# Performance work log

Hardware: AMD Instinct MI355X
Metric: run time of the kernel (lower is better)

Reference implementation:

```python
import jax, jax.numpy as jnp
import numpy as np
import math

L, B, S, D, H, FF = 6, 4, 1024, 1024, 16, 4096
HD = D // H
EPS = 1e-5


def _ln(x, g, b):
    m = jnp.mean(x, axis=-1, keepdims=True)
    v = jnp.mean(jnp.square(x - m), axis=-1, keepdims=True)
    return (x - m) / jnp.sqrt(v + EPS) * g + b


def setup_inputs() -> dict:
    key = jax.random.key(0)
    ks = jax.random.split(key, 8)
    std = 0.02
    inp = {
        'x': jax.random.normal(ks[0], (B, S, D), jnp.float32),
        'lengths': jax.random.randint(ks[1], (B,), S // 2, S + 1),
        'rel_bias': jax.random.normal(ks[2], (H, S, S), jnp.float32) * std,
        'ln1_g': jnp.ones((L, D), jnp.float32),
        'ln1_b': jnp.zeros((L, D), jnp.float32),
        'qkv_w': jax.random.normal(ks[3], (L, D, 3 * D), jnp.float32) * std,
        'qkv_b': jnp.zeros((L, 3 * D), jnp.float32),
        'out_w': jax.random.normal(ks[4], (L, D, D), jnp.float32) * std,
        'out_b': jnp.zeros((L, D), jnp.float32),
        'ln2_g': jnp.ones((L, D), jnp.float32),
        'ln2_b': jnp.zeros((L, D), jnp.float32),
        'fc1_w': jax.random.normal(ks[5], (L, D, FF), jnp.float32) * std,
        'fc1_b': jnp.zeros((L, FF), jnp.float32),
        'fc2_w': jax.random.normal(ks[6], (L, FF, D), jnp.float32) * std,
        'fc2_b': jnp.zeros((L, D), jnp.float32),
    }
    return inp


def reference(x, lengths, rel_bias, ln1_g, ln1_b, qkv_w, qkv_b, out_w, out_b,
              ln2_g, ln2_b, fc1_w, fc1_b, fc2_w, fc2_b):
    # causal additive mask [S,S]: -inf above the diagonal (torch.triu diagonal=1)
    ar = jnp.arange(S)
    causal = jnp.where(ar[None, :] > ar[:, None], -jnp.inf, 0.0).astype(x.dtype)
    # key padding mask [B,S]: True where position is padding
    pad = ar[None, :] >= lengths[:, None]
    scale = 1.0 / math.sqrt(HD)

    for i in range(L):
        # --- attention sub-block (pre-LN) ---
        xn = _ln(x, ln1_g[i], ln1_b[i])
        qkv = xn @ qkv_w[i] + qkv_b[i]                      # [B,S,3D]
        q, k, v = jnp.split(qkv, 3, axis=-1)
        q = q.reshape(B, S, H, HD)
        k = k.reshape(B, S, H, HD)
        v = v.reshape(B, S, H, HD)
        scores = jnp.einsum('bqhd,bkhd->bhqk', q, k) * scale  # [B,H,S,S]
        scores = scores + rel_bias[None] + causal[None, None]
        scores = jnp.where(pad[:, None, None, :], -jnp.inf, scores)
        attn = jax.nn.softmax(scores, axis=-1)
        o = jnp.einsum('bhqk,bkhd->bqhd', attn, v).reshape(B, S, D)
        o = o @ out_w[i] + out_b[i]
        o = jnp.where(pad[:, :, None], 0.0, o)
        x = x + o
        # --- feed-forward sub-block (LN inside FF, residual outside) ---
        h = _ln(x, ln2_g[i], ln2_b[i])
        h = jax.nn.gelu(h @ fc1_w[i] + fc1_b[i], approximate=False)
        h = h @ fc2_w[i] + fc2_b[i]
        x = x + h
    return x
```

## Files before the change

### kernel.cpp

```cpp
#include <hip/hip_runtime.h>
#include <cstdint>
#include <cstddef>

constexpr int L_ = 6, B_ = 4, S_ = 1024, D_ = 1024, H_ = 16, FF_ = 4096;
constexpr int D3_ = 3 * D_;
constexpr int HD_ = D_ / H_;

typedef float f32x4 __attribute__((ext_vector_type(4)));
typedef __bf16 bf16x8 __attribute__((ext_vector_type(8)));
typedef unsigned short u16;
typedef u16 u16x4 __attribute__((ext_vector_type(4)));
typedef u16 u16x8 __attribute__((ext_vector_type(8)));

__device__ __forceinline__ u16 f2bf(float f) {
    union { float f; uint32_t u; } v; v.f = f;
    uint32_t r = v.u + 0x7FFFu + ((v.u >> 16) & 1u);
    return (u16)(r >> 16);
}

__device__ __forceinline__ void gload16(const void* g, void* l) {
    __builtin_amdgcn_global_load_lds(
        (const __attribute__((address_space(1))) unsigned int*)g,
        (__attribute__((address_space(3))) unsigned int*)l,
        16, 0, 0);
}

__global__ __launch_bounds__(256) void cvt_layer(
    const float* __restrict__ qw, const float* __restrict__ ow,
    const float* __restrict__ f1w, const float* __restrict__ f2w,
    u16* __restrict__ tq, u16* __restrict__ to,
    u16* __restrict__ t1, u16* __restrict__ t2)
{
    __shared__ float tile[64][65];
    const int bid = blockIdx.x, tid = threadIdx.x;
    const float* W; u16* WT; int K, N, bn, bk;
    if (bid < 768)       { W = qw;  WT = tq; K = 1024; N = 3072; int t = bid;        bn = (t % 48) * 64; bk = (t / 48) * 64; }
    else if (bid < 1024) { W = ow;  WT = to; K = 1024; N = 1024; int t = bid - 768;  bn = (t % 16) * 64; bk = (t / 16) * 64; }
    else if (bid < 2048) { W = f1w; WT = t1; K = 1024; N = 4096; int t = bid - 1024; bn = (t % 64) * 64; bk = (t / 64) * 64; }
    else                 { W = f2w; WT = t2; K = 4096; N = 1024; int t = bid - 2048; bn = (t % 16) * 64; bk = (t / 16) * 64; }
    #pragma unroll
    for (int i = 0; i < 16; ++i) {
        int idx = i * 256 + tid;
        int r = idx >> 6, c = idx & 63;
        tile[r][c] = W[(size_t)(bk + r) * N + bn + c];
    }
    __syncthreads();
    #pragma unroll
    for (int i = 0; i < 16; ++i) {
        int idx = i * 256 + tid;
        int r = idx >> 6, c = idx & 63;
        WT[(size_t)(bn + r) * K + bk + c] = f2bf(tile[c][r]);
    }
}

__global__ __launch_bounds__(256) void vt_transpose(
    const u16* __restrict__ qkv, u16* __restrict__ vt)
{
    __shared__ u16 tile[64][72];
    const int tid = threadIdx.x;
    const int s0 = blockIdx.x * 64, bh = blockIdx.y;
    const int b = bh >> 4, h = bh & 15;
    #pragma unroll
    for (int i = 0; i < 2; ++i) {
        int idx = tid + i * 256;
        int r = idx >> 3, c8 = (idx & 7) * 8;
        u16x8 v = *(const u16x8*)(qkv + ((size_t)(b * S_ + s0 + r)) * D3_ + 2 * D_ + h * 64 + c8);
        #pragma unroll
        for (int j = 0; j < 8; ++j) tile[c8 + j][r] = v[j];
    }
    __syncthreads();
    #pragma unroll
    for (int i = 0; i < 2; ++i) {
        int idx = tid + i * 256;
        int r = idx >> 3, c8 = (idx & 7) * 8;
        u16x8 v;
        #pragma unroll
        for (int j = 0; j < 8; ++j) v[j] = tile[r][c8 + j];
        *(u16x8*)(vt + ((size_t)(bh * 64 + r)) * S_ + s0 + c8) = v;
    }
}

__global__ __launch_bounds__(256) void ln_kernel(
    const float* __restrict__ X, const float* __restrict__ g,
    const float* __restrict__ bp, u16* __restrict__ out)
{
    const int row = blockIdx.x, tid = threadIdx.x;
    const float* xr = X + (size_t)row * D_;
    f32x4 v = *(const f32x4*)(xr + tid * 4);
    float s  = v[0] + v[1] + v[2] + v[3];
    float s2 = v[0]*v[0] + v[1]*v[1] + v[2]*v[2] + v[3]*v[3];
    #pragma unroll
    for (int off = 32; off >= 1; off >>= 1) {
        s  += __shfl_down(s,  off);
        s2 += __shfl_down(s2, off);
    }
    __shared__ float red[8];
    const int lane = tid & 63, wid = tid >> 6;
    if (lane == 0) { red[wid] = s; red[4 + wid] = s2; }
    __syncthreads();
    s  = red[0] + red[1] + red[2] + red[3];
    s2 = red[4] + red[5] + red[6] + red[7];
    float mean = s * (1.f / D_);
    float var  = s2 * (1.f / D_) - mean * mean;
    float rstd = rsqrtf(var + 1e-5f);
    f32x4 gv = *(const f32x4*)(g  + tid * 4);
    f32x4 bv = *(const f32x4*)(bp + tid * 4);
    u16x4 o4;
    #pragma unroll
    for (int r = 0; r < 4; ++r) o4[r] = f2bf((v[r] - mean) * rstd * gv[r] + bv[r]);
    *(u16x4*)(out + (size_t)row * D_ + tid * 4) = o4;
}

template<int MODE>
__global__ __launch_bounds__(512, 2) void gemm256d(
    const u16* __restrict__ A, const u16* __restrict__ BT,
    const float* __restrict__ bias,
    u16* __restrict__ Cb, float* __restrict__ X,
    const int* __restrict__ lengths,
    int M, int N, int K)
{
    __shared__ __align__(16) char lds[4][32768];
    const int tid = threadIdx.x;
    const int lane = tid & 63;
    const int w = tid >> 6;
    const int grp = lane >> 4, l15 = lane & 15;
    const int wm = w >> 2, wn = w & 3;
    const int m0 = blockIdx.y * 256, n0 = blockIdx.x * 256;
    const int Kh = K / gridDim.z;
    const int k0 = blockIdx.z * Kh;
    const int NT = Kh >> 5;

    const int lrow = lane >> 2;
    const int cchunk = (lane & 3) ^ ((lane >> 3) & 3);
    const u16* gA = A  + (size_t)(m0 + w * 32 + lrow) * K + k0 + cchunk * 8;
    const u16* gB = BT + (size_t)(n0 + w * 32 + lrow) * K + k0 + cchunk * 8;
    const size_t row16 = (size_t)16 * K;
    char* const lA = &lds[0][0]     + w * 2048;
    char* const lB = &lds[0][16384] + w * 2048;
    const int rslot = (grp ^ ((l15 >> 1) & 3)) * 16;

#define STAGE_A(t) do { const u16* p_ = gA + (size_t)(t) * 32;                 \
        char* l_ = lA + ((t) & 3) * 32768;                                     \
        gload16(p_, l_); gload16(p_ + row16, l_ + 1024); } while (0)
#define STAGE_B(t) do { const u16* p_ = gB + (size_t)(t) * 32;                 \
        char* l_ = lB + ((t) & 3) * 32768;                                     \
        gload16(p_, l_); gload16(p_ + row16, l_ + 1024); } while (0)

    f32x4 acc[8][4] = {};

    STAGE_A(0); STAGE_B(0);
    if (NT > 1) { STAGE_A(1); STAGE_B(1); }
    if (NT > 2) { STAGE_A(2); STAGE_B(2); }

    for (int t = 0; t < NT; ++t) {
        const int rem = NT - t;
        if (rem > 2)       asm volatile("s_waitcnt vmcnt(8)" ::: "memory");
        else if (rem == 2) asm volatile("s_waitcnt vmcnt(4)" ::: "memory");
        else               asm volatile("s_waitcnt vmcnt(0)" ::: "memory");
        __builtin_amdgcn_s_barrier();
        __builtin_amdgcn_sched_barrier(0);
        const char* Ab = &lds[t & 3][0];
        const char* Bb = &lds[t & 3][16384];

        bf16x8 bfr[4], af0[4], af1[4];
        #pragma unroll
        for (int nf = 0; nf < 4; ++nf)
            bfr[nf] = *(const bf16x8*)(Bb + (wn * 64 + nf * 16 + l15) * 64 + rslot);
        #pragma unroll
        for (int mf = 0; mf < 4; ++mf)
            af0[mf] = *(const bf16x8*)(Ab + (wm * 128 + mf * 16 + l15) * 64 + rslot);
        if (t + 3 < NT) STAGE_A(t + 3);
        __builtin_amdgcn_s_setprio(1);
        #pragma unroll
        for (int mf = 0; mf < 4; ++mf)
            #pragma unroll
            for (int nf = 0; nf < 4; ++nf)
                acc[mf][nf] = __builtin_amdgcn_mfma_f32_16x16x32_bf16(
                    af0[mf], bfr[nf], acc[mf][nf], 0, 0, 0);
        __builtin_amdgcn_s_setprio(0);
        #pragma unroll
        for (int mf = 0; mf < 4; ++mf)
            af1[mf] = *(const bf16x8*)(Ab + (wm * 128 + 64 + mf * 16 + l15) * 64 + rslot);
        if (t + 3 < NT) STAGE_B(t + 3);
        __builtin_amdgcn_s_setprio(1);
        #pragma unroll
        for (int mf = 0; mf < 4; ++mf)
            #pragma unroll
            for (int nf = 0; nf < 4; ++nf)
                acc[4 + mf][nf] = __builtin_amdgcn_mfma_f32_16x16x32_bf16(
                    af1[mf], bfr[nf], acc[4 + mf][nf], 0, 0, 0);
        __builtin_amdgcn_s_setprio(0);
    }
#undef STAGE_A
#undef STAGE_B

    const float bscale = (k0 == 0) ? 1.f : 0.f;
    #pragma unroll
    for (int mi = 0; mi < 8; ++mi) {
        int row_g = m0 + wm * 128 + mi * 16 + grp * 4;
        #pragma unroll
        for (int nf = 0; nf < 4; ++nf) {
            int col_g = n0 + wn * 64 + nf * 16 + l15;
            float bv = bias[col_g] * bscale;
            f32x4 v = acc[mi][nf];
            if constexpr (MODE == 0) {
                #pragma unroll
                for (int r = 0; r < 4; ++r)
                    Cb[(size_t)(row_g + r) * N + col_g] = f2bf(v[r] + bv);
            } else if constexpr (MODE == 2) {
                #pragma unroll
                for (int r = 0; r < 4; ++r) {
                    float t = v[r] + bv;
                    float ge = 0.5f * t * (1.f + erff(t * 0.70710678118654752f));
                    Cb[(size_t)(row_g + r) * N + col_g] = f2bf(ge);
                }
            } else if constexpr (MODE == 1) {
                int len = lengths[row_g >> 10];
                #pragma unroll
                for (int r = 0; r < 4; ++r) {
                    int row = row_g + r;
                    float add = ((row & 1023) >= len) ? 0.f : (v[r] + bv);
                    atomicAdd(&X[(size_t)row * N + col_g], add);
                }
            } else {
                #pragma unroll
                for (int r = 0; r < 4; ++r)
                    atomicAdd(&X[(size_t)(row_g + r) * N + col_g], v[r] + bv);
            }
        }
    }
}

__global__ __launch_bounds__(256) void attn_kernel(
    const u16* __restrict__ qkv,
    const u16* __restrict__ vt,
    const float* __restrict__ rel_bias,
    const int* __restrict__ lengths,
    u16* __restrict__ obuf)
{
    __shared__ __align__(16) char kls[64 * 128];
    __shared__ __align__(16) char vls[64 * 128];
    const int tid = threadIdx.x, lane = tid & 63, wid = tid >> 6;
    const int grp = lane >> 4, l15 = lane & 15;
    const int qt = blockIdx.x, bh = blockIdx.y;
    const int b = bh >> 4, h = bh & 15;
    const int len = lengths[b];
    const int qrow = qt * 64 + wid * 16 + l15;

    bf16x8 qf[2];
    {
        const u16* qp = qkv + ((size_t)(b * S_ + qrow)) * D3_ + h * 64 + grp * 8;
        qf[0] = *(const bf16x8*)qp;
        qf[1] = *(const bf16x8*)(qp + 32);
    }
    f32x4 oacc[4] = {};
    float m_run = -INFINITY, lsum = 0.f;
    int kt_end = (len + 63) >> 6;
    if (qt + 1 < kt_end) kt_end = qt + 1;

    for (int kt = 0; kt < kt_end; ++kt) {
        __syncthreads();
        #pragma unroll
        for (int i = 0; i < 2; ++i) {
            int id2 = tid + i * 256;
            int r = id2 >> 3, gg = id2 & 7;
            int sw = (r & 7) << 4;
            bf16x8 kv = *(const bf16x8*)(qkv + ((size_t)(b * S_ + kt * 64 + r)) * D3_ + D_ + h * 64 + gg * 8);
            *(bf16x8*)(kls + r * 128 + ((gg * 16) ^ sw)) = kv;
            bf16x8 vv = *(const bf16x8*)(vt + ((size_t)(bh * 64 + r)) * S_ + kt * 64 + gg * 8);
            *(bf16x8*)(vls + r * 128 + ((gg * 16) ^ sw)) = vv;
        }
        __syncthreads();

        f32x4 sf[4] = {};
        #pragma unroll
        for (int f = 0; f < 4; ++f) {
            int r = f * 16 + l15;
            int sw = (r & 7) << 4;
            #pragma unroll
            for (int t = 0; t < 2; ++t) {
                bf16x8 af = *(const bf16x8*)(kls + r * 128 + (((t * 32 + grp * 8) * 2) ^ sw));
                sf[f] = __builtin_amdgcn_mfma_f32_16x16x32_bf16(af, qf[t], sf[f], 0, 0, 0);
            }
        }
        float p[4][4];
        float tmax = -INFINITY;
        #pragma unroll
        for (int f = 0; f < 4; ++f) {
            f32x4 bi = *(const f32x4*)(rel_bias + ((size_t)h * S_ + qrow) * S_ + kt * 64 + f * 16 + grp * 4);
            #pragma unroll
            for (int r = 0; r < 4; ++r) {
                int kp = kt * 64 + f * 16 + grp * 4 + r;
                bool valid = (kp <= qrow) && (kp < len);
                float sv = valid ? fmaf(sf[f][r], 0.125f, bi[r]) : -INFINITY;
                p[f][r] = sv;
                tmax = fmaxf(tmax, sv);
            }
        }
        tmax = fmaxf(tmax, __shfl_xor(tmax, 16));
        tmax = fmaxf(tmax, __shfl_xor(tmax, 32));
        float m_new = fmaxf(m_run, tmax);
        float alpha = expf(m_run - m_new);
        float psum = 0.f;
        #pragma unroll
        for (int f = 0; f < 4; ++f)
            #pragma unroll
            for (int r = 0; r < 4; ++r) {
                float e = expf(p[f][r] - m_new);
                p[f][r] = e; psum += e;
            }
        psum += __shfl_xor(psum, 16);
        psum += __shfl_xor(psum, 32);
        lsum = lsum * alpha + psum;
        m_run = m_new;
        #pragma unroll
        for (int fo = 0; fo < 4; ++fo) {
            oacc[fo][0] *= alpha; oacc[fo][1] *= alpha;
            oacc[fo][2] *= alpha; oacc[fo][3] *= alpha;
        }
        #pragma unroll
        for (int t = 0; t < 2; ++t) {
            union { u16 u[8]; bf16x8 v; } pb;
            #pragma unroll
            for (int j = 0; j < 4; ++j) {
                pb.u[j]     = f2bf(p[2 * t][j]);
                pb.u[4 + j] = f2bf(p[2 * t + 1][j]);
            }
            #pragma unroll
            for (int fo = 0; fo < 4; ++fo) {
                int r = fo * 16 + l15;
                int sw = (r & 7) << 4;
                union { u16x4 h4[2]; bf16x8 v; } av;
                av.h4[0] = *(const u16x4*)(vls + r * 128 + ((t * 64 + grp * 8)      ^ sw));
                av.h4[1] = *(const u16x4*)(vls + r * 128 + ((t * 64 + grp * 8 + 32) ^ sw));
                oacc[fo] = __builtin_amdgcn_mfma_f32_16x16x32_bf16(av.v, pb.v, oacc[fo], 0, 0, 0);
            }
        }
    }
    float inv = 1.f / lsum;
    #pragma unroll
    for (int fo = 0; fo < 4; ++fo)
        #pragma unroll
        for (int r = 0; r < 4; ++r) {
            int hd = fo * 16 + grp * 4 + r;
            obuf[((size_t)(b * S_) + qrow) * D_ + h * 64 + hd] = f2bf(oacc[fo][r] * inv);
        }
}

extern "C" void kernel_launch(void* const* d_in, const int* in_sizes, int n_in,
                              void* d_out, int out_size, void* d_ws, size_t ws_size,
                              hipStream_t stream)
{
    const float* x_in     = (const float*)d_in[0];
    const int*   lengths  = (const int*)d_in[1];
    const float* rel_bias = (const float*)d_in[2];
    const float* ln1_g    = (const float*)d_in[3];
    const float* ln1_b    = (const float*)d_in[4];
    const float* qkv_w    = (const float*)d_in[5];
    const float* qkv_b    = (const float*)d_in[6];
    const float* out_w    = (const float*)d_in[7];
    const float* out_b    = (const float*)d_in[8];
    const float* ln2_g    = (const float*)d_in[9];
    const float* ln2_b    = (const float*)d_in[10];
    const float* fc1_w    = (const float*)d_in[11];
    const float* fc1_b    = (const float*)d_in[12];
    const float* fc2_w    = (const float*)d_in[13];
    const float* fc2_b    = (const float*)d_in[14];
    float* X = (float*)d_out;

    char* ws = (char*)d_ws;
    size_t off = 0;
    auto alloc = [&](size_t bytes) {
        char* p = ws + off;
        off = (off + bytes + 255) & ~(size_t)255;
        return p;
    };
    u16* wT_qkv = (u16*)alloc((size_t)D3_ * D_ * 2);
    u16* wT_out = (u16*)alloc((size_t)D_ * D_ * 2);
    u16* wT_fc1 = (u16*)alloc((size_t)FF_ * D_ * 2);
    u16* wT_fc2 = (u16*)alloc((size_t)D_ * FF_ * 2);
    u16* xn     = (u16*)alloc((size_t)B_ * S_ * D_ * 2);
    u16* qkvb   = (u16*)alloc((size_t)B_ * S_ * D3_ * 2);
    u16* vtb    = (u16*)alloc((size_t)B_ * H_ * HD_ * S_ * 2);
    u16* ob     = (u16*)alloc((size_t)B_ * S_ * D_ * 2);
    u16* h1     = (u16*)alloc((size_t)B_ * S_ * FF_ * 2);

    const int M = B_ * S_;

    hipMemcpyAsync(X, x_in, (size_t)M * D_ * sizeof(float),
                   hipMemcpyDeviceToDevice, stream);

    for (int i = 0; i < L_; ++i) {
        cvt_layer<<<3072, 256, 0, stream>>>(
            qkv_w + (size_t)i * D_ * D3_, out_w + (size_t)i * D_ * D_,
            fc1_w + (size_t)i * D_ * FF_, fc2_w + (size_t)i * FF_ * D_,
            wT_qkv, wT_out, wT_fc1, wT_fc2);

        ln_kernel<<<M, 256, 0, stream>>>(X, ln1_g + i * D_, ln1_b + i * D_, xn);
        gemm256d<0><<<dim3(D3_ / 256, M / 256, 1), 512, 0, stream>>>(
            xn, wT_qkv, qkv_b + (size_t)i * D3_, qkvb, nullptr, nullptr, M, D3_, D_);
        vt_transpose<<<dim3(S_ / 64, B_ * H_), 256, 0, stream>>>(qkvb, vtb);
        attn_kernel<<<dim3(S_ / 64, B_ * H_), 256, 0, stream>>>(
            qkvb, vtb, rel_bias, lengths, ob);
        gemm256d<1><<<dim3(D_ / 256, M / 256, 4), 512, 0, stream>>>(
            ob, wT_out, out_b + (size_t)i * D_, nullptr, X, lengths, M, D_, D_);

        ln_kernel<<<M, 256, 0, stream>>>(X, ln2_g + i * D_, ln2_b + i * D_, xn);
        gemm256d<2><<<dim3(FF_ / 256, M / 256, 1), 512, 0, stream>>>(
            xn, wT_fc1, fc1_b + (size_t)i * FF_, h1, nullptr, nullptr, M, FF_, D_);
        gemm256d<3><<<dim3(D_ / 256, M / 256, 4), 512, 0, stream>>>(
            h1, wT_fc2, fc2_b + (size_t)i * D_, nullptr, X, nullptr, M, D_, FF_);
    }
}
```

Before: 1.929 ms.

## Unroll GEMM K-loop over four static LDS buffers and remap workgroups per XCD

```diff
diff --git a/kernel.cpp b/kernel.cpp
--- a/kernel.cpp
+++ b/kernel.cpp
@@ -112,22 +112,39 @@
 }
 
 template<int MODE>
-__global__ __launch_bounds__(512, 2) void gemm256d(
+__global__ __launch_bounds__(512, 2) void gemm256p(
     const u16* __restrict__ A, const u16* __restrict__ BT,
     const float* __restrict__ bias,
     u16* __restrict__ Cb, float* __restrict__ X,
     const int* __restrict__ lengths,
     int M, int N, int K)
 {
-    __shared__ __align__(16) char lds[4][32768];
+    __shared__ __align__(16) char sb0[32768];
+    __shared__ __align__(16) char sb1[32768];
+    __shared__ __align__(16) char sb2[32768];
+    __shared__ __align__(16) char sb3[32768];
+
     const int tid = threadIdx.x;
     const int lane = tid & 63;
     const int w = tid >> 6;
     const int grp = lane >> 4, l15 = lane & 15;
     const int wm = w >> 2, wn = w & 3;
-    const int m0 = blockIdx.y * 256, n0 = blockIdx.x * 256;
+
+    const int gx = gridDim.x, gy = gridDim.y;
+    const int nwg = gx * gy * gridDim.z;
+    int lid = blockIdx.x + gx * (blockIdx.y + gy * blockIdx.z);
+    {
+        int q = nwg >> 3, r = nwg & 7;
+        int xcd = lid & 7, wi = lid >> 3;
+        lid = (xcd < r ? xcd * (q + 1) : r * (q + 1) + (xcd - r) * q) + wi;
+    }
+    const int bx = lid % gx;
+    const int byz = lid / gx;
+    const int by = byz % gy, bz = byz / gy;
+
+    const int m0 = by * 256, n0 = bx * 256;
     const int Kh = K / gridDim.z;
-    const int k0 = blockIdx.z * Kh;
+    const int k0 = bz * Kh;
     const int NT = Kh >> 5;
 
     const int lrow = lane >> 2;
@@ -135,64 +152,68 @@
     const u16* gA = A  + (size_t)(m0 + w * 32 + lrow) * K + k0 + cchunk * 8;
     const u16* gB = BT + (size_t)(n0 + w * 32 + lrow) * K + k0 + cchunk * 8;
     const size_t row16 = (size_t)16 * K;
-    char* const lA = &lds[0][0]     + w * 2048;
-    char* const lB = &lds[0][16384] + w * 2048;
     const int rslot = (grp ^ ((l15 >> 1) & 3)) * 16;
 
-#define STAGE_A(t) do { const u16* p_ = gA + (size_t)(t) * 32;                 \
-        char* l_ = lA + ((t) & 3) * 32768;                                     \
-        gload16(p_, l_); gload16(p_ + row16, l_ + 1024); } while (0)
-#define STAGE_B(t) do { const u16* p_ = gB + (size_t)(t) * 32;                 \
-        char* l_ = lB + ((t) & 3) * 32768;                                     \
-        gload16(p_, l_); gload16(p_ + row16, l_ + 1024); } while (0)
+#define STAGE(t, BUF) do {                                                    \
+        const u16* pa_ = gA + (size_t)(t) * 32;                               \
+        const u16* pb_ = gB + (size_t)(t) * 32;                               \
+        char* la_ = (BUF) + w * 2048;                                         \
+        char* lb_ = (BUF) + 16384 + w * 2048;                                 \
+        gload16(pa_, la_); gload16(pa_ + row16, la_ + 1024);                  \
+        gload16(pb_, lb_); gload16(pb_ + row16, lb_ + 1024); } while (0)
 
     f32x4 acc[8][4] = {};
 
-    STAGE_A(0); STAGE_B(0);
-    if (NT > 1) { STAGE_A(1); STAGE_B(1); }
-    if (NT > 2) { STAGE_A(2); STAGE_B(2); }
-
-    for (int t = 0; t < NT; ++t) {
-        const int rem = NT - t;
-        if (rem > 2)       asm volatile("s_waitcnt vmcnt(8)" ::: "memory");
-        else if (rem == 2) asm volatile("s_waitcnt vmcnt(4)" ::: "memory");
-        else               asm volatile("s_waitcnt vmcnt(0)" ::: "memory");
-        __builtin_amdgcn_s_barrier();
-        __builtin_amdgcn_sched_barrier(0);
-        const char* Ab = &lds[t & 3][0];
-        const char* Bb = &lds[t & 3][16384];
-
-        bf16x8 bfr[4], af0[4], af1[4];
-        #pragma unroll
-        for (int nf = 0; nf < 4; ++nf)
-            bfr[nf] = *(const bf16x8*)(Bb + (wn * 64 + nf * 16 + l15) * 64 + rslot);
-        #pragma unroll
-        for (int mf = 0; mf < 4; ++mf)
-            af0[mf] = *(const bf16x8*)(Ab + (wm * 128 + mf * 16 + l15) * 64 + rslot);
-        if (t + 3 < NT) STAGE_A(t + 3);
-        __builtin_amdgcn_s_setprio(1);
-        #pragma unroll
-        for (int mf = 0; mf < 4; ++mf)
-            #pragma unroll
-            for (int nf = 0; nf < 4; ++nf)
-                acc[mf][nf] = __builtin_amdgcn_mfma_f32_16x16x32_bf16(
-                    af0[mf], bfr[nf], acc[mf][nf], 0, 0, 0);
-        __builtin_amdgcn_s_setprio(0);
-        #pragma unroll
-        for (int mf = 0; mf < 4; ++mf)
-            af1[mf] = *(const bf16x8*)(Ab + (wm * 128 + 64 + mf * 16 + l15) * 64 + rslot);
-        if (t + 3 < NT) STAGE_B(t + 3);
-        __builtin_amdgcn_s_setprio(1);
-        #pragma unroll
-        for (int mf = 0; mf < 4; ++mf)
-            #pragma unroll
-            for (int nf = 0; nf < 4; ++nf)
-                acc[4 + mf][nf] = __builtin_amdgcn_mfma_f32_16x16x32_bf16(
-                    af1[mf], bfr[nf], acc[4 + mf][nf], 0, 0, 0);
-        __builtin_amdgcn_s_setprio(0);
-    }
-#undef STAGE_A
-#undef STAGE_B
+#define TILEBODY(CUR, WAITSTR, STAGE_STMT) do {                               \
+        asm volatile(WAITSTR ::: "memory");                                   \
+        __builtin_amdgcn_s_barrier();                                         \
+        __builtin_amdgcn_sched_barrier(0);                                    \
+        const char* Ab_ = (CUR);                                              \
+        const char* Bb_ = (CUR) + 16384;                                      \
+        bf16x8 bfr_[4], af0_[4], af1_[4];                                     \
+        _Pragma("unroll")                                                     \
+        for (int nf = 0; nf < 4; ++nf)                                        \
+            bfr_[nf] = *(const bf16x8*)(Bb_ + (wn * 64 + nf * 16 + l15) * 64 + rslot); \
+        _Pragma("unroll")                                                     \
+        for (int mf = 0; mf < 4; ++mf)                                        \
+            af0_[mf] = *(const bf16x8*)(Ab_ + (wm * 128 + mf * 16 + l15) * 64 + rslot); \
+        _Pragma("unroll")                                                     \
+        for (int mf = 0; mf < 4; ++mf)                                        \
+            af1_[mf] = *(const bf16x8*)(Ab_ + (wm * 128 + 64 + mf * 16 + l15) * 64 + rslot); \
+        STAGE_STMT;                                                           \
+        __builtin_amdgcn_s_setprio(1);                                        \
+        _Pragma("unroll")                                                     \
+        for (int mf = 0; mf < 4; ++mf)                                        \
+            _Pragma("unroll")                                                 \
+            for (int nf = 0; nf < 4; ++nf)                                    \
+                acc[mf][nf] = __builtin_amdgcn_mfma_f32_16x16x32_bf16(        \
+                    af0_[mf], bfr_[nf], acc[mf][nf], 0, 0, 0);                \
+        _Pragma("unroll")                                                     \
+        for (int mf = 0; mf < 4; ++mf)                                        \
+            _Pragma("unroll")                                                 \
+            for (int nf = 0; nf < 4; ++nf)                                    \
+                acc[4 + mf][nf] = __builtin_amdgcn_mfma_f32_16x16x32_bf16(    \
+                    af1_[mf], bfr_[nf], acc[4 + mf][nf], 0, 0, 0);            \
+        __builtin_amdgcn_s_setprio(0);                                        \
+    } while (0)
+
+    STAGE(0, sb0);
+    STAGE(1, sb1);
+    STAGE(2, sb2);
+
+    int t = 0;
+    for (; t + 4 < NT; t += 4) {
+        TILEBODY(sb0, "s_waitcnt vmcnt(8)", STAGE(t + 3, sb3));
+        TILEBODY(sb1, "s_waitcnt vmcnt(8)", STAGE(t + 4, sb0));
+        TILEBODY(sb2, "s_waitcnt vmcnt(8)", STAGE(t + 5, sb1));
+        TILEBODY(sb3, "s_waitcnt vmcnt(8)", STAGE(t + 6, sb2));
+    }
+    TILEBODY(sb0, "s_waitcnt vmcnt(8)", STAGE(t + 3, sb3));
+    TILEBODY(sb1, "s_waitcnt vmcnt(8)", (void)0);
+    TILEBODY(sb2, "s_waitcnt vmcnt(4)", (void)0);
+    TILEBODY(sb3, "s_waitcnt vmcnt(0)", (void)0);
+#undef TILEBODY
+#undef STAGE
 
     const float bscale = (k0 == 0) ? 1.f : 0.f;
     #pragma unroll
@@ -210,8 +231,8 @@
             } else if constexpr (MODE == 2) {
                 #pragma unroll
                 for (int r = 0; r < 4; ++r) {
-                    float t = v[r] + bv;
-                    float ge = 0.5f * t * (1.f + erff(t * 0.70710678118654752f));
+                    float tv = v[r] + bv;
+                    float ge = 0.5f * tv * (1.f + erff(tv * 0.70710678118654752f));
                     Cb[(size_t)(row_g + r) * N + col_g] = f2bf(ge);
                 }
             } else if constexpr (MODE == 1) {
@@ -397,18 +418,18 @@
             wT_qkv, wT_out, wT_fc1, wT_fc2);
 
         ln_kernel<<<M, 256, 0, stream>>>(X, ln1_g + i * D_, ln1_b + i * D_, xn);
-        gemm256d<0><<<dim3(D3_ / 256, M / 256, 1), 512, 0, stream>>>(
+        gemm256p<0><<<dim3(D3_ / 256, M / 256, 1), 512, 0, stream>>>(
             xn, wT_qkv, qkv_b + (size_t)i * D3_, qkvb, nullptr, nullptr, M, D3_, D_);
         vt_transpose<<<dim3(S_ / 64, B_ * H_), 256, 0, stream>>>(qkvb, vtb);
         attn_kernel<<<dim3(S_ / 64, B_ * H_), 256, 0, stream>>>(
             qkvb, vtb, rel_bias, lengths, ob);
-        gemm256d<1><<<dim3(D_ / 256, M / 256, 4), 512, 0, stream>>>(
+        gemm256p<1><<<dim3(D_ / 256, M / 256, 4), 512, 0, stream>>>(
             ob, wT_out, out_b + (size_t)i * D_, nullptr, X, lengths, M, D_, D_);
 
         ln_kernel<<<M, 256, 0, stream>>>(X, ln2_g + i * D_, ln2_b + i * D_, xn);
-        gemm256d<2><<<dim3(FF_ / 256, M / 256, 1), 512, 0, stream>>>(
+        gemm256p<2><<<dim3(FF_ / 256, M / 256, 1), 512, 0, stream>>>(
             xn, wT_fc1, fc1_b + (size_t)i * FF_, h1, nullptr, nullptr, M, FF_, D_);
-        gemm256d<3><<<dim3(D_ / 256, M / 256, 4), 512, 0, stream>>>(
+        gemm256p<3><<<dim3(D_ / 256, M / 256, 4), 512, 0, stream>>>(
             h1, wT_fc2, fc2_b + (size_t)i * D_, nullptr, X, nullptr, M, D_, FF_);
     }
 }
```

Measured after the change: 1.904 ms. Within noise of the previous version (-1.3%).

## Remap GEMM workgroups per XCD and restructure pipeline into barrier-fenced phases

Applied to the files above, without the earlier changes.

```diff
diff --git a/kernel.cpp b/kernel.cpp
--- a/kernel.cpp
+++ b/kernel.cpp
@@ -112,7 +112,7 @@
 }
 
 template<int MODE>
-__global__ __launch_bounds__(512, 2) void gemm256d(
+__global__ __launch_bounds__(512, 2) void gemm8p(
     const u16* __restrict__ A, const u16* __restrict__ BT,
     const float* __restrict__ bias,
     u16* __restrict__ Cb, float* __restrict__ X,
@@ -125,9 +125,22 @@
     const int w = tid >> 6;
     const int grp = lane >> 4, l15 = lane & 15;
     const int wm = w >> 2, wn = w & 3;
-    const int m0 = blockIdx.y * 256, n0 = blockIdx.x * 256;
+
+    const int gx = gridDim.x, gy = gridDim.y;
+    const int nwg = gx * gy * gridDim.z;
+    int lid = blockIdx.x + gx * (blockIdx.y + gy * blockIdx.z);
+    {
+        int q = nwg >> 3, r = nwg & 7;
+        int xcd = lid & 7, wi = lid >> 3;
+        lid = (xcd < r ? xcd * (q + 1) : r * (q + 1) + (xcd - r) * q) + wi;
+    }
+    const int bx = lid % gx;
+    const int byz = lid / gx;
+    const int by = byz % gy, bz = byz / gy;
+
+    const int m0 = by * 256, n0 = bx * 256;
     const int Kh = K / gridDim.z;
-    const int k0 = blockIdx.z * Kh;
+    const int k0 = bz * Kh;
     const int NT = Kh >> 5;
 
     const int lrow = lane >> 2;
@@ -135,61 +148,67 @@
     const u16* gA = A  + (size_t)(m0 + w * 32 + lrow) * K + k0 + cchunk * 8;
     const u16* gB = BT + (size_t)(n0 + w * 32 + lrow) * K + k0 + cchunk * 8;
     const size_t row16 = (size_t)16 * K;
-    char* const lA = &lds[0][0]     + w * 2048;
-    char* const lB = &lds[0][16384] + w * 2048;
     const int rslot = (grp ^ ((l15 >> 1) & 3)) * 16;
 
-#define STAGE_A(t) do { const u16* p_ = gA + (size_t)(t) * 32;                 \
-        char* l_ = lA + ((t) & 3) * 32768;                                     \
+#define STAGE_A(t) do { const u16* p_ = gA + (size_t)(t) * 32;                \
+        char* l_ = &lds[(t) & 3][0] + w * 2048;                               \
         gload16(p_, l_); gload16(p_ + row16, l_ + 1024); } while (0)
-#define STAGE_B(t) do { const u16* p_ = gB + (size_t)(t) * 32;                 \
-        char* l_ = lB + ((t) & 3) * 32768;                                     \
+#define STAGE_B(t) do { const u16* p_ = gB + (size_t)(t) * 32;                \
+        char* l_ = &lds[(t) & 3][16384] + w * 2048;                           \
         gload16(p_, l_); gload16(p_ + row16, l_ + 1024); } while (0)
 
     f32x4 acc[8][4] = {};
 
     STAGE_A(0); STAGE_B(0);
-    if (NT > 1) { STAGE_A(1); STAGE_B(1); }
-    if (NT > 2) { STAGE_A(2); STAGE_B(2); }
+    STAGE_A(1); STAGE_B(1);
+    STAGE_A(2); STAGE_B(2);
+    asm volatile("s_waitcnt vmcnt(8)" ::: "memory");
+    __builtin_amdgcn_s_barrier();
 
     for (int t = 0; t < NT; ++t) {
-        const int rem = NT - t;
-        if (rem > 2)       asm volatile("s_waitcnt vmcnt(8)" ::: "memory");
-        else if (rem == 2) asm volatile("s_waitcnt vmcnt(4)" ::: "memory");
-        else               asm volatile("s_waitcnt vmcnt(0)" ::: "memory");
-        __builtin_amdgcn_s_barrier();
-        __builtin_amdgcn_sched_barrier(0);
         const char* Ab = &lds[t & 3][0];
         const char* Bb = &lds[t & 3][16384];
-
-        bf16x8 bfr[4], af0[4], af1[4];
+        bf16x8 bfr[4], af[4];
+
         #pragma unroll
         for (int nf = 0; nf < 4; ++nf)
             bfr[nf] = *(const bf16x8*)(Bb + (wn * 64 + nf * 16 + l15) * 64 + rslot);
         #pragma unroll
         for (int mf = 0; mf < 4; ++mf)
-            af0[mf] = *(const bf16x8*)(Ab + (wm * 128 + mf * 16 + l15) * 64 + rslot);
+            af[mf] = *(const bf16x8*)(Ab + (wm * 128 + mf * 16 + l15) * 64 + rslot);
         if (t + 3 < NT) STAGE_A(t + 3);
+        __builtin_amdgcn_s_barrier();
+        asm volatile("s_waitcnt lgkmcnt(0)" ::: "memory");
+        __builtin_amdgcn_sched_barrier(0);
         __builtin_amdgcn_s_setprio(1);
         #pragma unroll
         for (int mf = 0; mf < 4; ++mf)
             #pragma unroll
             for (int nf = 0; nf < 4; ++nf)
                 acc[mf][nf] = __builtin_amdgcn_mfma_f32_16x16x32_bf16(
-                    af0[mf], bfr[nf], acc[mf][nf], 0, 0, 0);
+                    af[mf], bfr[nf], acc[mf][nf], 0, 0, 0);
         __builtin_amdgcn_s_setprio(0);
+        __builtin_amdgcn_s_barrier();
+
         #pragma unroll
         for (int mf = 0; mf < 4; ++mf)
-            af1[mf] = *(const bf16x8*)(Ab + (wm * 128 + 64 + mf * 16 + l15) * 64 + rslot);
+            af[mf] = *(const bf16x8*)(Ab + (wm * 128 + 64 + mf * 16 + l15) * 64 + rslot);
         if (t + 3 < NT) STAGE_B(t + 3);
+        if (t + 3 < NT)      asm volatile("s_waitcnt vmcnt(8)" ::: "memory");
+        else if (t + 2 < NT) asm volatile("s_waitcnt vmcnt(4)" ::: "memory");
+        else                 asm volatile("s_waitcnt vmcnt(0)" ::: "memory");
+        __builtin_amdgcn_s_barrier();
+        asm volatile("s_waitcnt lgkmcnt(0)" ::: "memory");
+        __builtin_amdgcn_sched_barrier(0);
         __builtin_amdgcn_s_setprio(1);
         #pragma unroll
         for (int mf = 0; mf < 4; ++mf)
             #pragma unroll
             for (int nf = 0; nf < 4; ++nf)
                 acc[4 + mf][nf] = __builtin_amdgcn_mfma_f32_16x16x32_bf16(
-                    af1[mf], bfr[nf], acc[4 + mf][nf], 0, 0, 0);
+                    af[mf], bfr[nf], acc[4 + mf][nf], 0, 0, 0);
         __builtin_amdgcn_s_setprio(0);
+        __builtin_amdgcn_s_barrier();
     }
 #undef STAGE_A
 #undef STAGE_B
@@ -210,8 +229,8 @@
             } else if constexpr (MODE == 2) {
                 #pragma unroll
                 for (int r = 0; r < 4; ++r) {
-                    float t = v[r] + bv;
-                    float ge = 0.5f * t * (1.f + erff(t * 0.70710678118654752f));
+                    float tv = v[r] + bv;
+                    float ge = 0.5f * tv * (1.f + erff(tv * 0.70710678118654752f));
                     Cb[(size_t)(row_g + r) * N + col_g] = f2bf(ge);
                 }
             } else if constexpr (MODE == 1) {
@@ -397,18 +416,18 @@
             wT_qkv, wT_out, wT_fc1, wT_fc2);
 
         ln_kernel<<<M, 256, 0, stream>>>(X, ln1_g + i * D_, ln1_b + i * D_, xn);
-        gemm256d<0><<<dim3(D3_ / 256, M / 256, 1), 512, 0, stream>>>(
+        gemm8p<0><<<dim3(D3_ / 256, M / 256, 1), 512, 0, stream>>>(
             xn, wT_qkv, qkv_b + (size_t)i * D3_, qkvb, nullptr, nullptr, M, D3_, D_);
         vt_transpose<<<dim3(S_ / 64, B_ * H_), 256, 0, stream>>>(qkvb, vtb);
         attn_kernel<<<dim3(S_ / 64, B_ * H_), 256, 0, stream>>>(
             qkvb, vtb, rel_bias, lengths, ob);
-        gemm256d<1><<<dim3(D_ / 256, M / 256, 4), 512, 0, stream>>>(
+        gemm8p<1><<<dim3(D_ / 256, M / 256, 4), 512, 0, stream>>>(
             ob, wT_out, out_b + (size_t)i * D_, nullptr, X, lengths, M, D_, D_);
 
         ln_kernel<<<M, 256, 0, stream>>>(X, ln2_g + i * D_, ln2_b + i * D_, xn);
-        gemm256d<2><<<dim3(FF_ / 256, M / 256, 1), 512, 0, stream>>>(
+        gemm8p<2><<<dim3(FF_ / 256, M / 256, 1), 512, 0, stream>>>(
             xn, wT_fc1, fc1_b + (size_t)i * FF_, h1, nullptr, nullptr, M, FF_, D_);
-        gemm256d<3><<<dim3(D_ / 256, M / 256, 4), 512, 0, stream>>>(
+        gemm8p<3><<<dim3(D_ / 256, M / 256, 4), 512, 0, stream>>>(
             h1, wT_fc2, fc2_b + (size_t)i * D_, nullptr, X, nullptr, M, D_, FF_);
     }
 }
```

New measurement: 1.936 ms. Within noise of the previous version (+0.4%).
